# Kernel tuning notes

Measured on AMD Instinct MI355X. Metric: run time of the kernel, lower is better.

Reference implementation:

```python
import jax, jax.numpy as jnp
import numpy as np

E, H = 1024, 16
B, N = 4, 2048
D = E // H

def setup_inputs() -> dict:
    key = jax.random.key(0)
    ks = jax.random.split(key, 5)
    s = 1.0 / np.sqrt(E)
    return {
        "x": jax.random.normal(ks[0], (B, N, E), dtype=jnp.float32),
        "Wqkv": jax.random.normal(ks[1], (E, 3 * E), dtype=jnp.float32) * s,
        "bqkv": jnp.zeros((3 * E,), dtype=jnp.float32),
        "Wproj": jax.random.normal(ks[2], (E, E), dtype=jnp.float32) * s,
        "bproj": jnp.zeros((E,), dtype=jnp.float32),
    }

def reference(x, Wqkv, bqkv, Wproj, bproj):
    b, n, e = x.shape
    qkv = x @ Wqkv + bqkv  # [b, n, 3e]
    # torch rearrange 'b n (h d qkv) -> qkv b h n d': last dim splits as (h, d, 3)
    qkv = qkv.reshape(b, n, H, D, 3)
    qkv = jnp.transpose(qkv, (4, 0, 2, 1, 3))  # [3, b, h, n, d]
    q, k, v = qkv[0], qkv[1], qkv[2]
    # NOTE: module scales by 1/sqrt(e) (full embed dim), faithfully reproduced
    att = jax.nn.softmax(jnp.einsum('bhqd,bhkd->bhqk', q, k) / jnp.sqrt(jnp.float32(E)), axis=-1)
    out = jnp.einsum('bhqk,bhkd->bhqd', att, v)  # dropout is identity in eval
    out = jnp.transpose(out, (0, 2, 1, 3)).reshape(b, n, e)  # 'b h n d -> b n (h d)'
    return out @ Wproj + bproj
```

## Files before the change

kernel.cpp:

```cpp
#include <hip/hip_runtime.h>
#include <stdint.h>

typedef unsigned short u16;
typedef __attribute__((ext_vector_type(8))) short short8;
typedef __attribute__((ext_vector_type(4))) float f32x4;

#define LOG2E 1.44269504088896340736f
#define CS (0.03125f * LOG2E)
#define BB 4
#define NN 2048
#define EE 1024
#define HH 16
#define DD 64
#define MM 8192
#define C3 3072

#if __has_builtin(__builtin_amdgcn_exp2f)
#define EXP2(x) __builtin_amdgcn_exp2f(x)
#else
#define EXP2(x) exp2f(x)
#endif

__device__ __forceinline__ u16 f2bf(float f) {
  union { float f; unsigned u; } v; v.f = f;
  unsigned r = v.u + 0x7fffu + ((v.u >> 16) & 1u);
  return (u16)(r >> 16);
}

#if __has_builtin(__builtin_amdgcn_cvt_pk_bf16_f32)
typedef __attribute__((ext_vector_type(2))) __bf16 bf16x2;
__device__ __forceinline__ unsigned pk2(float a, float b) {
  union { bf16x2 v; unsigned u; } c;
  c.v = __builtin_amdgcn_cvt_pk_bf16_f32(a, b);
  return c.u;
}
#else
__device__ __forceinline__ unsigned pk2(float a, float b) {
  union { float f; unsigned u; } x, y; x.f = a; y.f = b;
  return ((x.u + 0x8000u) >> 16) | ((y.u + 0x8000u) & 0xffff0000u);
}
#endif

__device__ __forceinline__ void async16(const void* g, void* l) {
  __builtin_amdgcn_global_load_lds((const __attribute__((address_space(1))) void*)g,
                                   (__attribute__((address_space(3))) void*)l,
                                   16, 0, 0);
}

__device__ __forceinline__ int vperm(int t) {
  return (t & 0x23) | ((t & 8) << 1) | ((t & 4) << 1) | ((t & 16) >> 2);
}

__global__ __launch_bounds__(256) void prep_kernel(const float* __restrict__ x, u16* __restrict__ xb,
                                                   const float* __restrict__ Wqkv, u16* __restrict__ WqkvT,
                                                   const float* __restrict__ Wproj, u16* __restrict__ WprojT) {
  __shared__ float tile[32][33];
  const int bid = blockIdx.x;
  if (bid < 8192) {
    int i = (bid * 256 + threadIdx.x) * 4;
    float4 v = *(const float4*)(x + i);
    ushort4 o; o.x = f2bf(v.x); o.y = f2bf(v.y); o.z = f2bf(v.z); o.w = f2bf(v.w);
    *(ushort4*)(xb + i) = o;
    return;
  }
  const int permute = bid < 11264 ? 1 : 0;
  const float* W = permute ? Wqkv : Wproj;
  u16* Wt = permute ? WqkvT : WprojT;
  const int ncols = permute ? C3 : EE;
  const int t = permute ? bid - 8192 : bid - 11264;
  const int nbx = permute ? 96 : 32;
  const int c0 = (t % nbx) * 32, k0 = (t / nbx) * 32;
  const int tx = threadIdx.x & 31, ty = threadIdx.x >> 5;
#pragma unroll
  for (int r = 0; r < 32; r += 8)
    tile[ty + r][tx] = W[(size_t)(k0 + ty + r) * ncols + c0 + tx];
  __syncthreads();
#pragma unroll
  for (int r = 0; r < 32; r += 8) {
    int c = c0 + ty + r;
    int cp = c;
    if (permute) {
      int tt = c % 3, hh = c / 192, d = (c / 3) % 64;
      cp = tt * 1024 + hh * 64 + d;
    }
    Wt[(size_t)cp * EE + k0 + tx] = f2bf(tile[tx][ty + r]);
  }
}

template <int KDIM>
__device__ __forceinline__ void gemm_core(const u16* __restrict__ A, const u16* __restrict__ Bt,
                                          int m0, int n0, u16* As, u16* Bs, f32x4 acc[4][4]) {
  const int tid = threadIdx.x;
  const int lane = tid & 63, wave = tid >> 6;
  const int q = lane >> 4, r16 = lane & 15;
  const int wrow = (wave >> 1) * 64, wcol = (wave & 1) * 64;
#pragma unroll
  for (int i = 0; i < 4; i++)
#pragma unroll
    for (int j = 0; j < 4; j++) acc[i][j] = (f32x4){0.f, 0.f, 0.f, 0.f};

  for (int k0 = 0; k0 < KDIM; k0 += 64) {
#pragma unroll
    for (int i = 0; i < 4; i++) {
      int c = i * 256 + tid;
      int ks = c >> 9, rem = c & 511, row = rem >> 2, k8 = rem & 3;
      async16(A + (size_t)(m0 + row) * KDIM + k0 + ks * 32 + k8 * 8, &As[c * 8]);
    }
#pragma unroll
    for (int i = 0; i < 4; i++) {
      int c = i * 256 + tid;
      int ks = c >> 9, rem = c & 511, row = rem >> 2, k8 = rem & 3;
      async16(Bt + (size_t)(n0 + row) * KDIM + k0 + ks * 32 + k8 * 8, &Bs[c * 8]);
    }
    __syncthreads();
#pragma unroll
    for (int ks = 0; ks < 2; ks++) {
      short8 af[4], bf[4];
#pragma unroll
      for (int i = 0; i < 4; i++)
        af[i] = *(const short8*)&As[ks * 4096 + (wrow + i * 16 + r16) * 32 + q * 8];
#pragma unroll
      for (int i = 0; i < 4; i++)
        bf[i] = *(const short8*)&Bs[ks * 4096 + (wcol + i * 16 + r16) * 32 + q * 8];
#pragma unroll
      for (int i = 0; i < 4; i++)
#pragma unroll
        for (int j = 0; j < 4; j++)
          acc[i][j] = __builtin_amdgcn_mfma_f32_16x16x32_bf16(af[i], bf[j], acc[i][j], 0, 0, 0);
    }
    __syncthreads();
  }
}


__global__ __launch_bounds__(256) void gemm_qkv(const u16* __restrict__ Xb, const u16* __restrict__ Wt,
                                                const float* __restrict__ bqkv, u16* __restrict__ Qb,
                                                u16* __restrict__ KVt) {
  __shared__ __align__(16) u16 As[128 * 64];
  __shared__ __align__(16) u16 Bs[128 * 64];
  f32x4 acc[4][4];
  const int m0 = blockIdx.y * 128, n0 = blockIdx.x * 128;
  gemm_core<EE>(Xb, Wt, m0, n0, As, Bs, acc);
  const int tid = threadIdx.x, lane = tid & 63, wave = tid >> 6;
  const int q = lane >> 4, r16 = lane & 15;
  const int wrow = (wave >> 1) * 64, wcol = (wave & 1) * 64;
  const int t = (n0 + wcol) >> 10;
  const int b = (m0 + wrow) >> 11;
#pragma unroll
  for (int ci = 0; ci < 4; ci++) {
    const int cp = n0 + wcol + ci * 16 + r16;
    const int hh = (cp >> 6) & 15, d = cp & 63;
    const float bias = bqkv[hh * 192 + d * 3 + t];
    if (t == 0) {
#pragma unroll
      for (int ri = 0; ri < 4; ri++)
#pragma unroll
        for (int r = 0; r < 4; r++) {
          const int m = m0 + wrow + ri * 16 + q * 4 + r;
          Qb[((size_t)(b * 16 + hh) * 2048 + (m & 2047)) * 64 + d] = f2bf((acc[ri][ci][r] + bias) * CS);
        }
    } else if (t == 1) {
      const size_t bhbase = (size_t)(b * 16 + hh) * 32;
      const size_t dpart = (size_t)(d >> 5) * 2048 + ((d >> 3) & 3) * 128 + (d & 7);
#pragma unroll
      for (int ri = 0; ri < 4; ri++)
#pragma unroll
        for (int r = 0; r < 4; r++) {
          const int key = (m0 + wrow + ri * 16 + q * 4 + r) & 2047;
          KVt[(bhbase + (key >> 6)) * 8192 + dpart + ((key >> 4) & 3) * 512 + (key & 15) * 8] =
              f2bf(acc[ri][ci][r] + bias);
        }
    } else {
      const size_t bhbase = (size_t)(b * 16 + hh) * 32;
      const int dpart = (d >> 4) * 512 + (d & 15) * 8;
#pragma unroll
      for (int ri = 0; ri < 4; ri++) {
        const int nb = (m0 + wrow + ri * 16 + q * 4) & 2047;
        const int sb = vperm(nb & 63);
        ushort4 w;
        w.x = f2bf(acc[ri][ci][0] + bias);
        w.y = f2bf(acc[ri][ci][1] + bias);
        w.z = f2bf(acc[ri][ci][2] + bias);
        w.w = f2bf(acc[ri][ci][3] + bias);
        *(ushort4*)&KVt[(bhbase + (nb >> 6)) * 8192 + 4096 + (sb >> 5) * 2048 +
                        ((sb >> 3) & 3) * 128 + dpart + (sb & 7)] = w;
      }
    }
  }
}

__global__ __launch_bounds__(256) void gemm_proj(const u16* __restrict__ Ob, const u16* __restrict__ Wt,
                                                 const float* __restrict__ bp, float* __restrict__ out) {
  __shared__ __align__(16) u16 As[128 * 64];
  __shared__ __align__(16) u16 Bs[128 * 64];
  f32x4 acc[4][4];
  const int m0 = blockIdx.y * 128, n0 = blockIdx.x * 128;
  gemm_core<EE>(Ob, Wt, m0, n0, As, Bs, acc);
  const int tid = threadIdx.x, lane = tid & 63, wave = tid >> 6;
  const int q = lane >> 4, r16 = lane & 15;
  const int wrow = (wave >> 1) * 64, wcol = (wave & 1) * 64;
#pragma unroll
  for (int ci = 0; ci < 4; ci++) {
    const int col = n0 + wcol + ci * 16 + r16;
    const float bias = bp[col];
#pragma unroll
    for (int ri = 0; ri < 4; ri++)
#pragma unroll
      for (int r = 0; r < 4; r++) {
        const int m = m0 + wrow + ri * 16 + q * 4 + r;
        out[(size_t)m * EE + col] = acc[ri][ci][r] + bias;
      }
  }
}

__global__ __launch_bounds__(256, 4) void attn_kernel(const u16* __restrict__ Qg, const u16* __restrict__ KVg,
                                                      u16* __restrict__ Ob) {
  __shared__ __align__(16) u16 KVd[2][8192];
  const int tid = threadIdx.x, lane = tid & 63, wave = tid >> 6;
  const int q = lane >> 4, r16 = lane & 15;
  const int id = blockIdx.x + 16 * blockIdx.y;
  const int g = id & 7, s = id >> 3;
  const int bh = g * 8 + (s >> 4);
  const int q0 = (s & 15) * 128;
  const u16* Qp = Qg + ((size_t)bh * NN + q0) * DD;
  const u16* KVp = KVg + (size_t)bh * (32 * 8192);

  short8 qf[2][2];
#pragma unroll
  for (int nj = 0; nj < 2; nj++)
#pragma unroll
    for (int ks = 0; ks < 2; ks++)
      qf[nj][ks] = *(const short8*)(Qp + (wave * 32 + nj * 16 + r16) * 64 + ks * 32 + q * 8);

#pragma unroll
  for (int i = 0; i < 4; i++) {
    int c = i * 256 + tid;
    async16(KVp + c * 8, &KVd[0][c * 8]);
  }
  __syncthreads();

  f32x4 o[2][4];
  f32x4 ol[2];
#pragma unroll
  for (int i = 0; i < 2; i++) {
    ol[i] = (f32x4){0.f, 0.f, 0.f, 0.f};
#pragma unroll
    for (int j = 0; j < 4; j++) o[i][j] = (f32x4){0.f, 0.f, 0.f, 0.f};
  }
  const short8 ones = {16256, 16256, 16256, 16256, 16256, 16256, 16256, 16256};

  for (int j = 0; j < 32; j++) {
    const int buf = j & 1;
    if (j < 31) {
      const u16* src = KVp + (size_t)(j + 1) * 8192;
#pragma unroll
      for (int i = 0; i < 4; i++) {
        int c = i * 256 + tid;
        async16(src + c * 8, &KVd[buf ^ 1][c * 8]);
      }
    }

    f32x4 st[4][2];
#pragma unroll
    for (int mi = 0; mi < 4; mi++)
#pragma unroll
      for (int nj = 0; nj < 2; nj++) st[mi][nj] = (f32x4){0.f, 0.f, 0.f, 0.f};
#pragma unroll
    for (int ks = 0; ks < 2; ks++) {
      short8 kf[4];
#pragma unroll
      for (int mi = 0; mi < 4; mi++)
        kf[mi] = *(const short8*)&KVd[buf][ks * 2048 + mi * 512 + lane * 8];
#pragma unroll
      for (int mi = 0; mi < 4; mi++)
#pragma unroll
        for (int nj = 0; nj < 2; nj++)
          st[mi][nj] = __builtin_amdgcn_mfma_f32_16x16x32_bf16(kf[mi], qf[nj][ks], st[mi][nj], 0, 0, 0);
    }

    uint2 pka[4][2];
#pragma unroll
    for (int mi = 0; mi < 4; mi++)
#pragma unroll
      for (int nj = 0; nj < 2; nj++) {
        float p0 = EXP2(st[mi][nj][0]);
        float p1 = EXP2(st[mi][nj][1]);
        float p2 = EXP2(st[mi][nj][2]);
        float p3 = EXP2(st[mi][nj][3]);
        pka[mi][nj].x = pk2(p0, p1);
        pka[mi][nj].y = pk2(p2, p3);
      }

#pragma unroll
    for (int kp = 0; kp < 2; kp++) {
      short8 vf[4];
#pragma unroll
      for (int ci = 0; ci < 4; ci++)
        vf[ci] = *(const short8*)&KVd[buf][4096 + kp * 2048 + ci * 512 + lane * 8];
#pragma unroll
      for (int ri = 0; ri < 2; ri++) {
        union { uint4 u; short8 s; } a;
        a.u.x = pka[2 * kp][ri].x;
        a.u.y = pka[2 * kp][ri].y;
        a.u.z = pka[2 * kp + 1][ri].x;
        a.u.w = pka[2 * kp + 1][ri].y;
#pragma unroll
        for (int ci = 0; ci < 4; ci++)
          o[ri][ci] = __builtin_amdgcn_mfma_f32_16x16x32_bf16(a.s, vf[ci], o[ri][ci], 0, 0, 0);
        ol[ri] = __builtin_amdgcn_mfma_f32_16x16x32_bf16(a.s, ones, ol[ri], 0, 0, 0);
      }
    }

    __syncthreads();
  }

  const int b = bh >> 4, h = bh & 15;
#pragma unroll
  for (int ri = 0; ri < 2; ri++)
#pragma unroll
    for (int r = 0; r < 4; r++) {
      const float inv = 1.0f / ol[ri][r];
      const int n = q0 + wave * 32 + ri * 16 + q * 4 + r;
#pragma unroll
      for (int ci = 0; ci < 4; ci++) {
        const int d = ci * 16 + r16;
        Ob[((size_t)(b * NN + n)) * EE + h * 64 + d] = f2bf(o[ri][ci][r] * inv);
      }
    }
}


extern "C" void kernel_launch(void* const* d_in, const int* in_sizes, int n_in,
                              void* d_out, int out_size, void* d_ws, size_t ws_size,
                              hipStream_t stream) {
  const float* x     = (const float*)d_in[0];
  const float* Wqkv  = (const float*)d_in[1];
  const float* bqkv  = (const float*)d_in[2];
  const float* Wproj = (const float*)d_in[3];
  const float* bproj = (const float*)d_in[4];
  float* out = (float*)d_out;
  char* ws = (char*)d_ws;

  u16* Xb     = (u16*)(ws);
  u16* Ob     = Xb;
  u16* Qb     = (u16*)(ws + (size_t)(16 << 20));
  u16* KVt    = (u16*)(ws + (size_t)(32 << 20));
  u16* WqkvT  = (u16*)(ws + (size_t)(64 << 20));
  u16* WprojT = (u16*)(ws + (size_t)(72 << 20));

  prep_kernel<<<12288, 256, 0, stream>>>(x, Xb, Wqkv, WqkvT, Wproj, WprojT);
  gemm_qkv<<<dim3(24, 64), 256, 0, stream>>>(Xb, WqkvT, bqkv, Qb, KVt);
  attn_kernel<<<dim3(16, 64), 256, 0, stream>>>(Qb, KVt, Ob);
  gemm_proj<<<dim3(8, 64), 256, 0, stream>>>(Ob, WprojT, bproj, out);
}
```

Before: 276.7 us.

## Triple-buffer GEMM K-loop with async prefetch and enlarge QKV tile to 256 rows

```diff
diff --git a/kernel.cpp b/kernel.cpp
--- a/kernel.cpp
+++ b/kernel.cpp
@@ -87,65 +87,90 @@
   }
 }
 
-template <int KDIM>
+template <int KDIM, int MI>
 __device__ __forceinline__ void gemm_core(const u16* __restrict__ A, const u16* __restrict__ Bt,
-                                          int m0, int n0, u16* As, u16* Bs, f32x4 acc[4][4]) {
-  const int tid = threadIdx.x;
-  const int lane = tid & 63, wave = tid >> 6;
-  const int q = lane >> 4, r16 = lane & 15;
-  const int wrow = (wave >> 1) * 64, wcol = (wave & 1) * 64;
-#pragma unroll
-  for (int i = 0; i < 4; i++)
+                                          int m0, int n0, u16* As, u16* Bs, f32x4 (*acc)[4]) {
+  constexpr int L2M = (MI == 8) ? 3 : 2;
+  constexpr int ACH = MI * 128;
+  constexpr int ALD = MI / 2;
+  constexpr int ASZ = ACH * 8;
+  constexpr int NT = KDIM / 32;
+  const int tid = threadIdx.x, lane = tid & 63, wave = tid >> 6;
+  const int wm = wave >> 1, wn = wave & 1;
+
+#pragma unroll
+  for (int i = 0; i < MI; i++)
 #pragma unroll
     for (int j = 0; j < 4; j++) acc[i][j] = (f32x4){0.f, 0.f, 0.f, 0.f};
 
-  for (int k0 = 0; k0 < KDIM; k0 += 64) {
-#pragma unroll
-    for (int i = 0; i < 4; i++) {
+  auto stage = [&](int t, int slot) {
+    const u16* Ab = A + (size_t)m0 * KDIM + t * 32;
+    const u16* Bb = Bt + (size_t)n0 * KDIM + t * 32;
+#pragma unroll
+    for (int i = 0; i < ALD; i++) {
       int c = i * 256 + tid;
-      int ks = c >> 9, rem = c & 511, row = rem >> 2, k8 = rem & 3;
-      async16(A + (size_t)(m0 + row) * KDIM + k0 + ks * 32 + k8 * 8, &As[c * 8]);
-    }
-#pragma unroll
-    for (int i = 0; i < 4; i++) {
+      int r = c & 15, qc = (c >> 4) & 3, mi = (c >> 6) & (MI - 1), wmc = c >> (6 + L2M);
+      int row = (wmc * MI + mi) * 16 + r;
+      async16(Ab + (size_t)row * KDIM + qc * 8, &As[slot * ASZ + c * 8]);
+    }
+#pragma unroll
+    for (int i = 0; i < 2; i++) {
       int c = i * 256 + tid;
-      int ks = c >> 9, rem = c & 511, row = rem >> 2, k8 = rem & 3;
-      async16(Bt + (size_t)(n0 + row) * KDIM + k0 + ks * 32 + k8 * 8, &Bs[c * 8]);
-    }
-    __syncthreads();
-#pragma unroll
-    for (int ks = 0; ks < 2; ks++) {
-      short8 af[4], bf[4];
-#pragma unroll
-      for (int i = 0; i < 4; i++)
-        af[i] = *(const short8*)&As[ks * 4096 + (wrow + i * 16 + r16) * 32 + q * 8];
-#pragma unroll
-      for (int i = 0; i < 4; i++)
-        bf[i] = *(const short8*)&Bs[ks * 4096 + (wcol + i * 16 + r16) * 32 + q * 8];
-#pragma unroll
-      for (int i = 0; i < 4; i++)
-#pragma unroll
-        for (int j = 0; j < 4; j++)
-          acc[i][j] = __builtin_amdgcn_mfma_f32_16x16x32_bf16(af[i], bf[j], acc[i][j], 0, 0, 0);
-    }
-    __syncthreads();
-  }
-}
-
-
-__global__ __launch_bounds__(256) void gemm_qkv(const u16* __restrict__ Xb, const u16* __restrict__ Wt,
-                                                const float* __restrict__ bqkv, u16* __restrict__ Qb,
-                                                u16* __restrict__ KVt) {
-  __shared__ __align__(16) u16 As[128 * 64];
-  __shared__ __align__(16) u16 Bs[128 * 64];
-  f32x4 acc[4][4];
-  const int m0 = blockIdx.y * 128, n0 = blockIdx.x * 128;
-  gemm_core<EE>(Xb, Wt, m0, n0, As, Bs, acc);
+      int r = c & 15, qc = (c >> 4) & 3, ci = (c >> 6) & 3, wnc = c >> 8;
+      int row = (wnc * 4 + ci) * 16 + r;
+      async16(Bb + (size_t)row * KDIM + qc * 8, &Bs[slot * 4096 + c * 8]);
+    }
+  };
+
+  stage(0, 0);
+  stage(1, 1);
+  if constexpr (MI == 8) asm volatile("s_waitcnt vmcnt(6)" ::: "memory");
+  else                   asm volatile("s_waitcnt vmcnt(4)" ::: "memory");
+  __builtin_amdgcn_s_barrier();
+
+  for (int t = 0; t < NT; ++t) {
+    const int slot = t % 3;
+    if (t + 2 < NT) stage(t + 2, (t + 2) % 3);
+    short8 af[MI], bf[4];
+    const u16* Ar = As + slot * ASZ + (wm * (MI * 64) + lane) * 8;
+#pragma unroll
+    for (int mi = 0; mi < MI; mi++) af[mi] = *(const short8*)(Ar + mi * 512);
+    const u16* Br = Bs + slot * 4096 + (wn * 256 + lane) * 8;
+#pragma unroll
+    for (int ci = 0; ci < 4; ci++) bf[ci] = *(const short8*)(Br + ci * 512);
+    __builtin_amdgcn_s_setprio(1);
+#pragma unroll
+    for (int mi = 0; mi < MI; mi++)
+#pragma unroll
+      for (int ci = 0; ci < 4; ci++)
+        acc[mi][ci] = __builtin_amdgcn_mfma_f32_16x16x32_bf16(af[mi], bf[ci], acc[mi][ci], 0, 0, 0);
+    __builtin_amdgcn_s_setprio(0);
+    if (t + 2 < NT) {
+      if constexpr (MI == 8) asm volatile("s_waitcnt vmcnt(6)" ::: "memory");
+      else                   asm volatile("s_waitcnt vmcnt(4)" ::: "memory");
+      __builtin_amdgcn_s_barrier();
+    } else if (t + 1 < NT) {
+      asm volatile("s_waitcnt vmcnt(0)" ::: "memory");
+      __builtin_amdgcn_s_barrier();
+    }
+  }
+}
+
+
+__global__ __launch_bounds__(256, 2) void gemm_qkv(const u16* __restrict__ Xb, const u16* __restrict__ Wt,
+                                                   const float* __restrict__ bqkv, u16* __restrict__ Qb,
+                                                   u16* __restrict__ KVt) {
+  __shared__ __align__(16) u16 As[3 * 8192];
+  __shared__ __align__(16) u16 Bs[3 * 4096];
+  f32x4 acc[8][4];
+  const int m0 = blockIdx.y * 256, n0 = blockIdx.x * 128;
+  gemm_core<EE, 8>(Xb, Wt, m0, n0, As, Bs, acc);
   const int tid = threadIdx.x, lane = tid & 63, wave = tid >> 6;
   const int q = lane >> 4, r16 = lane & 15;
-  const int wrow = (wave >> 1) * 64, wcol = (wave & 1) * 64;
-  const int t = (n0 + wcol) >> 10;
-  const int b = (m0 + wrow) >> 11;
+  const int wm = wave >> 1, wn = wave & 1;
+  const int wrow = wm * 128, wcol = wn * 64;
+  const int t = n0 >> 10;
+  const int b = m0 >> 11;
 #pragma unroll
   for (int ci = 0; ci < 4; ci++) {
     const int cp = n0 + wcol + ci * 16 + r16;
@@ -153,35 +178,35 @@
     const float bias = bqkv[hh * 192 + d * 3 + t];
     if (t == 0) {
 #pragma unroll
-      for (int ri = 0; ri < 4; ri++)
+      for (int mi = 0; mi < 8; mi++)
 #pragma unroll
         for (int r = 0; r < 4; r++) {
-          const int m = m0 + wrow + ri * 16 + q * 4 + r;
-          Qb[((size_t)(b * 16 + hh) * 2048 + (m & 2047)) * 64 + d] = f2bf((acc[ri][ci][r] + bias) * CS);
+          const int m = m0 + wrow + mi * 16 + q * 4 + r;
+          Qb[((size_t)(b * 16 + hh) * 2048 + (m & 2047)) * 64 + d] = f2bf((acc[mi][ci][r] + bias) * CS);
         }
     } else if (t == 1) {
       const size_t bhbase = (size_t)(b * 16 + hh) * 32;
       const size_t dpart = (size_t)(d >> 5) * 2048 + ((d >> 3) & 3) * 128 + (d & 7);
 #pragma unroll
-      for (int ri = 0; ri < 4; ri++)
+      for (int mi = 0; mi < 8; mi++)
 #pragma unroll
         for (int r = 0; r < 4; r++) {
-          const int key = (m0 + wrow + ri * 16 + q * 4 + r) & 2047;
+          const int key = (m0 + wrow + mi * 16 + q * 4 + r) & 2047;
           KVt[(bhbase + (key >> 6)) * 8192 + dpart + ((key >> 4) & 3) * 512 + (key & 15) * 8] =
-              f2bf(acc[ri][ci][r] + bias);
+              f2bf(acc[mi][ci][r] + bias);
         }
     } else {
       const size_t bhbase = (size_t)(b * 16 + hh) * 32;
       const int dpart = (d >> 4) * 512 + (d & 15) * 8;
 #pragma unroll
-      for (int ri = 0; ri < 4; ri++) {
-        const int nb = (m0 + wrow + ri * 16 + q * 4) & 2047;
+      for (int mi = 0; mi < 8; mi++) {
+        const int nb = (m0 + wrow + mi * 16 + q * 4) & 2047;
         const int sb = vperm(nb & 63);
         ushort4 w;
-        w.x = f2bf(acc[ri][ci][0] + bias);
-        w.y = f2bf(acc[ri][ci][1] + bias);
-        w.z = f2bf(acc[ri][ci][2] + bias);
-        w.w = f2bf(acc[ri][ci][3] + bias);
+        w.x = f2bf(acc[mi][ci][0] + bias);
+        w.y = f2bf(acc[mi][ci][1] + bias);
+        w.z = f2bf(acc[mi][ci][2] + bias);
+        w.w = f2bf(acc[mi][ci][3] + bias);
         *(ushort4*)&KVt[(bhbase + (nb >> 6)) * 8192 + 4096 + (sb >> 5) * 2048 +
                         ((sb >> 3) & 3) * 128 + dpart + (sb & 7)] = w;
       }
@@ -189,13 +214,13 @@
   }
 }
 
-__global__ __launch_bounds__(256) void gemm_proj(const u16* __restrict__ Ob, const u16* __restrict__ Wt,
-                                                 const float* __restrict__ bp, float* __restrict__ out) {
-  __shared__ __align__(16) u16 As[128 * 64];
-  __shared__ __align__(16) u16 Bs[128 * 64];
+__global__ __launch_bounds__(256, 3) void gemm_proj(const u16* __restrict__ Ob, const u16* __restrict__ Wt,
+                                                    const float* __restrict__ bp, float* __restrict__ out) {
+  __shared__ __align__(16) u16 As[3 * 4096];
+  __shared__ __align__(16) u16 Bs[3 * 4096];
   f32x4 acc[4][4];
   const int m0 = blockIdx.y * 128, n0 = blockIdx.x * 128;
-  gemm_core<EE>(Ob, Wt, m0, n0, As, Bs, acc);
+  gemm_core<EE, 4>(Ob, Wt, m0, n0, As, Bs, acc);
   const int tid = threadIdx.x, lane = tid & 63, wave = tid >> 6;
   const int q = lane >> 4, r16 = lane & 15;
   const int wrow = (wave >> 1) * 64, wcol = (wave & 1) * 64;
@@ -204,11 +229,11 @@
     const int col = n0 + wcol + ci * 16 + r16;
     const float bias = bp[col];
 #pragma unroll
-    for (int ri = 0; ri < 4; ri++)
+    for (int mi = 0; mi < 4; mi++)
 #pragma unroll
       for (int r = 0; r < 4; r++) {
-        const int m = m0 + wrow + ri * 16 + q * 4 + r;
-        out[(size_t)m * EE + col] = acc[ri][ci][r] + bias;
+        const int m = m0 + wrow + mi * 16 + q * 4 + r;
+        out[(size_t)m * EE + col] = acc[mi][ci][r] + bias;
       }
   }
 }
@@ -349,7 +374,7 @@
   u16* WprojT = (u16*)(ws + (size_t)(72 << 20));
 
   prep_kernel<<<12288, 256, 0, stream>>>(x, Xb, Wqkv, WqkvT, Wproj, WprojT);
-  gemm_qkv<<<dim3(24, 64), 256, 0, stream>>>(Xb, WqkvT, bqkv, Qb, KVt);
+  gemm_qkv<<<dim3(24, 32), 256, 0, stream>>>(Xb, WqkvT, bqkv, Qb, KVt);
   attn_kernel<<<dim3(16, 64), 256, 0, stream>>>(Qb, KVt, Ob);
   gemm_proj<<<dim3(8, 64), 256, 0, stream>>>(Ob, WprojT, bproj, out);
 }
```

New measurement: 299.2 us. +8.1%, slower.
